# Kernel tuning notes

Measured on AMD Instinct MI355X. Metric: run time of the kernel, lower is better.

Reference implementation:

```python
import jax, jax.numpy as jnp
import numpy as np

EPS = 1e-5
NUM_HEADS = 16


def _layernorm(x, g, b):
    mu = jnp.mean(x, axis=-1, keepdims=True)
    var = jnp.mean(jnp.square(x - mu), axis=-1, keepdims=True)
    return (x - mu) * jax.lax.rsqrt(var + EPS) * g + b


def setup_inputs() -> dict:
    key = jax.random.key(0)
    ks = jax.random.split(key, 8)
    B, N, D, Hid = 2, 2048, 1024, 4096
    s = 0.02
    return {
        "x": jax.random.normal(ks[0], (B, N, D), dtype=jnp.float32),
        "w_qkv": jax.random.normal(ks[1], (D, 3 * D), dtype=jnp.float32) * s,
        "b_qkv": jnp.zeros((3 * D,), dtype=jnp.float32),
        "ln_g": jnp.ones((D,), dtype=jnp.float32),
        "ln_b": jnp.zeros((D,), dtype=jnp.float32),
        "w1": jax.random.normal(ks[2], (D, Hid), dtype=jnp.float32) * s,
        "b1": jnp.zeros((Hid,), dtype=jnp.float32),
        "w2": jax.random.normal(ks[3], (Hid, D), dtype=jnp.float32) * s,
        "b2": jnp.zeros((D,), dtype=jnp.float32),
    }


def reference(x, w_qkv, b_qkv, ln_g, ln_b, w1, b1, w2, b2):
    B, N, D = x.shape
    H = NUM_HEADS
    Dh = D // H

    # --- attention branch (pre-norm, shared LayerNorm params) ---
    xn = _layernorm(x, ln_g, ln_b)
    qkv = xn @ w_qkv + b_qkv                       # [B, N, 3D]
    qkv = qkv.reshape(B, N, 3, H, Dh).transpose(2, 0, 3, 1, 4)  # [3, B, H, N, Dh]
    q, k, v = qkv[0], qkv[1], qkv[2]
    # NOTE: original module applies NO 1/sqrt(Dh) scaling
    att = jax.nn.softmax(jnp.einsum('bhqd,bhkd->bhqk', q, k), axis=-1)
    o = jnp.einsum('bhqk,bhkd->bhqd', att, v)      # [B, H, N, Dh]
    # Faithful to source: raw reshape of [B, H, N, Dh] -> [B, N, D]
    # (the original code does NOT transpose heads back before merging)
    attn_out = o.reshape(B, N, D)
    x = x + attn_out

    # --- MLP branch ---
    xn2 = _layernorm(x, ln_g, ln_b)
    h = jax.nn.gelu(xn2 @ w1 + b1, approximate=False)
    mlp_out = h @ w2 + b2
    return x + mlp_out
```

## Files before the change

### kernel.cpp

```cpp
#include <hip/hip_runtime.h>
#include <cstdint>
#include <math.h>

typedef __attribute__((ext_vector_type(4))) float f32x4;
typedef __attribute__((ext_vector_type(8))) short bf16x8;
typedef unsigned short u16;
typedef __attribute__((ext_vector_type(4))) unsigned short u16x4;

#define LOG2E 1.44269504088896340736f

__device__ __forceinline__ u16 f2bf(float f) {
  uint32_t u = __builtin_bit_cast(uint32_t, f);
  u += 0x7FFFu + ((u >> 16) & 1u);
  return (u16)(u >> 16);
}

__device__ __forceinline__ void g2lds16(const void* g, void* l) {
  __builtin_amdgcn_global_load_lds((const __attribute__((address_space(1))) void*)g,
                                   (__attribute__((address_space(3))) void*)l, 16, 0, 0);
}

__device__ __forceinline__ float qsum16(float v) {
  v += __shfl_xor(v, 1);
  v += __shfl_xor(v, 2);
  v += __shfl_xor(v, 4);
  v += __shfl_xor(v, 8);
  return v;
}
__device__ __forceinline__ float wsum64(float v) {
  #pragma unroll
  for (int m = 32; m > 0; m >>= 1) v += __shfl_xor(v, m);
  return v;
}

__global__ void __launch_bounds__(256) transpose_f32_bf16(
    const float* __restrict__ in, u16* __restrict__ out, int R, int C) {
  __shared__ float tile[32][33];
  const int bx = blockIdx.x, by = blockIdx.y;
  const int tx = threadIdx.x & 31, ty = threadIdx.x >> 5;
  #pragma unroll
  for (int j = 0; j < 4; ++j)
    tile[ty + j * 8][tx] = in[(size_t)(by * 32 + ty + j * 8) * C + bx * 32 + tx];
  __syncthreads();
  #pragma unroll
  for (int j = 0; j < 4; ++j)
    out[(size_t)(bx * 32 + ty + j * 8) * R + by * 32 + tx] = f2bf(tile[tx][ty + j * 8]);
}

__global__ void __launch_bounds__(256) ln_kernel(
    const float* __restrict__ x, const float* __restrict__ g,
    const float* __restrict__ b, u16* __restrict__ out) {
  __shared__ float red[8];
  const int row = blockIdx.x, t = threadIdx.x, w = t >> 6;
  const float4 v = ((const float4*)(x + (size_t)row * 1024))[t];
  float s = v.x + v.y + v.z + v.w;
  s = wsum64(s);
  if ((t & 63) == 0) red[w] = s;
  __syncthreads();
  const float mean = (red[0] + red[1] + red[2] + red[3]) * (1.0f / 1024.0f);
  const float dx = v.x - mean, dy = v.y - mean, dz = v.z - mean, dw = v.w - mean;
  float s2 = dx * dx + dy * dy + dz * dz + dw * dw;
  s2 = wsum64(s2);
  if ((t & 63) == 0) red[4 + w] = s2;
  __syncthreads();
  const float rstd = rsqrtf((red[4] + red[5] + red[6] + red[7]) * (1.0f / 1024.0f) + 1e-5f);
  const float4 gv = ((const float4*)g)[t];
  const float4 bv = ((const float4*)b)[t];
  u16x4 o;
  o.x = f2bf(dx * rstd * gv.x + bv.x);
  o.y = f2bf(dy * rstd * gv.y + bv.y);
  o.z = f2bf(dz * rstd * gv.z + bv.z);
  o.w = f2bf(dw * rstd * gv.w + bv.w);
  ((u16x4*)(out + (size_t)row * 1024))[t] = o;
}

template <int EPI>
__global__ void __launch_bounds__(256, 2) gemm_bt(
    const u16* __restrict__ A, const u16* __restrict__ Bt,
    const float* __restrict__ bias, int M, int N, int K,
    u16* __restrict__ ob, const float* __restrict__ res, float* __restrict__ of) {
  __shared__ u16 As[128 * 32];
  __shared__ u16 Bs[128 * 32];
  const int t = threadIdx.x;
  const int w = t >> 6, l = t & 63;
  const int lq = l >> 4, lr = l & 15;
  const int sw = (lr >> 1) & 3;
  const int wm = w >> 1, wn = w & 1;
  const int row0 = blockIdx.x * 128, col0 = blockIdx.y * 128;
  f32x4 acc[4][4] = {};
  for (int k0 = 0; k0 < K; k0 += 32) {
    #pragma unroll
    for (int i = 0; i < 2; ++i) {
      int c = i * 256 + t;
      int row = c >> 2, cl = (c & 3) ^ ((row >> 1) & 3);
      g2lds16(A + (size_t)(row0 + row) * K + k0 + cl * 8,
              (char*)As + (i * 256 + w * 64) * 16);
    }
    #pragma unroll
    for (int i = 0; i < 2; ++i) {
      int c = i * 256 + t;
      int row = c >> 2, cl = (c & 3) ^ ((row >> 1) & 3);
      g2lds16(Bt + (size_t)(col0 + row) * K + k0 + cl * 8,
              (char*)Bs + (i * 256 + w * 64) * 16);
    }
    __syncthreads();
    bf16x8 af[4], bf[4];
    #pragma unroll
    for (int tm = 0; tm < 4; ++tm)
      af[tm] = *(const bf16x8*)&As[(wm * 64 + tm * 16 + lr) * 32 + (lq ^ sw) * 8];
    #pragma unroll
    for (int tn = 0; tn < 4; ++tn)
      bf[tn] = *(const bf16x8*)&Bs[(wn * 64 + tn * 16 + lr) * 32 + (lq ^ sw) * 8];
    #pragma unroll
    for (int tm = 0; tm < 4; ++tm)
      #pragma unroll
      for (int tn = 0; tn < 4; ++tn)
        acc[tm][tn] = __builtin_amdgcn_mfma_f32_16x16x32_bf16(af[tm], bf[tn], acc[tm][tn], 0, 0, 0);
    __syncthreads();
  }
  #pragma unroll
  for (int tm = 0; tm < 4; ++tm) {
    #pragma unroll
    for (int tn = 0; tn < 4; ++tn) {
      const int gcol = col0 + wn * 64 + tn * 16 + lr;
      const float bv = bias[gcol];
      float vals[4];
      #pragma unroll
      for (int r = 0; r < 4; ++r) vals[r] = acc[tm][tn][r] + bv;
      const int g0 = row0 + wm * 64 + tm * 16 + lq * 4;
      if (EPI == 0) {
        const int tsel = gcol >> 10, hh = (gcol >> 6) & 15, dh = gcol & 63;
        const int bb = g0 >> 11, n0 = g0 & 2047;
        if (tsel == 2) {
          u16x4 pk;
          pk.x = f2bf(vals[0]); pk.y = f2bf(vals[1]);
          pk.z = f2bf(vals[2]); pk.w = f2bf(vals[3]);
          *(u16x4*)&ob[8388608 + (size_t)((bb * 16 + hh) * 64 + dh) * 2048 + n0] = pk;
        } else {
          const float sc = (tsel == 0) ? LOG2E : 1.0f;
          const size_t base = (tsel ? 4194304u : 0u) +
                              (size_t)(bb * 16 + hh) * 2048 * 64 + dh;
          #pragma unroll
          for (int r = 0; r < 4; ++r)
            ob[base + (size_t)(n0 + r) * 64] = f2bf(vals[r] * sc);
        }
      } else if (EPI == 1) {
        #pragma unroll
        for (int r = 0; r < 4; ++r) {
          const float gelu = 0.5f * vals[r] * (1.0f + erff(vals[r] * 0.70710678118654752f));
          ob[(size_t)(g0 + r) * N + gcol] = f2bf(gelu);
        }
      } else {
        #pragma unroll
        for (int r = 0; r < 4; ++r) {
          const size_t idx = (size_t)(g0 + r) * N + gcol;
          of[idx] = res[idx] + vals[r];
        }
      }
    }
  }
}

__global__ void __launch_bounds__(256, 2) attn_kernel(
    const u16* __restrict__ q, const u16* __restrict__ k, const u16* __restrict__ vt,
    const float* __restrict__ x, float* __restrict__ x2) {
  __shared__ u16 Ks[128 * 64];
  __shared__ u16 Vs[64 * 128];
  __shared__ u16 Ps[4][16 * 136];
  const int t = threadIdx.x, w = t >> 6, l = t & 63;
  const int lq = l >> 4, lr = l & 15;
  const int sw = lr & 7;
  const int bh = blockIdx.y, qt = blockIdx.x;
  const size_t head = (size_t)bh * (2048 * 64);
  const u16* qh = q + head;
  const u16* kh = k + head;
  const u16* vth = vt + head;

  bf16x8 qf[2][2];
  #pragma unroll
  for (int tm = 0; tm < 2; ++tm)
    #pragma unroll
    for (int kk = 0; kk < 2; ++kk)
      qf[tm][kk] = *(const bf16x8*)&qh[(size_t)(qt * 128 + w * 32 + tm * 16 + lr) * 64 + kk * 32 + lq * 8];

  f32x4 o_acc[2][4] = {};
  float rsum[2][4] = {};
  u16* const pbase = &Ps[w][lq * 544 + lr];

  for (int kt = 0; kt < 16; ++kt) {
    #pragma unroll
    for (int i = 0; i < 4; ++i) {
      int c = i * 256 + t;
      int row = c >> 3, cl = (c & 7) ^ (row & 7);
      g2lds16(kh + (size_t)(kt * 128 + row) * 64 + cl * 8,
              (char*)Ks + (i * 256 + w * 64) * 16);
    }
    #pragma unroll
    for (int i = 0; i < 4; ++i) {
      int c = i * 256 + t;
      int row = c >> 4, cl = (c & 15) ^ (row & 7);
      g2lds16(vth + (size_t)row * 2048 + kt * 128 + cl * 8,
              (char*)Vs + (i * 256 + w * 64) * 16);
    }
    __syncthreads();
    bf16x8 kf[8][2];
    #pragma unroll
    for (int tn = 0; tn < 8; ++tn)
      #pragma unroll
      for (int kk = 0; kk < 2; ++kk)
        kf[tn][kk] = *(const bf16x8*)&Ks[(tn * 16 + lr) * 64 + ((kk * 4 + lq) ^ sw) * 8];
    #pragma unroll
    for (int tm = 0; tm < 2; ++tm) {
      f32x4 s_acc[8] = {};
      #pragma unroll
      for (int tn = 0; tn < 8; ++tn)
        #pragma unroll
        for (int kk = 0; kk < 2; ++kk)
          s_acc[tn] = __builtin_amdgcn_mfma_f32_16x16x32_bf16(qf[tm][kk], kf[tn][kk], s_acc[tn], 0, 0, 0);
      #pragma unroll
      for (int tn = 0; tn < 8; ++tn)
        #pragma unroll
        for (int r = 0; r < 4; ++r) {
          const float p = __builtin_amdgcn_exp2f(s_acc[tn][r]);
          rsum[tm][r] += p;
          pbase[r * 136 + tn * 16] = (u16)(__builtin_bit_cast(uint32_t, p) >> 16);
        }
      #pragma unroll
      for (int kk2 = 0; kk2 < 4; ++kk2) {
        const bf16x8 pf = *(const bf16x8*)&Ps[w][lr * 136 + kk2 * 32 + lq * 8];
        #pragma unroll
        for (int tn = 0; tn < 4; ++tn) {
          const bf16x8 vf = *(const bf16x8*)&Vs[(tn * 16 + lr) * 128 + ((kk2 * 4 + lq) ^ sw) * 8];
          o_acc[tm][tn] = __builtin_amdgcn_mfma_f32_16x16x32_bf16(pf, vf, o_acc[tm][tn], 0, 0, 0);
        }
      }
    }
    __syncthreads();
  }
  float inv[2][4];
  #pragma unroll
  for (int tm = 0; tm < 2; ++tm)
    #pragma unroll
    for (int r = 0; r < 4; ++r)
      inv[tm][r] = 1.0f / qsum16(rsum[tm][r]);
  const int bb = bh >> 4, hh = bh & 15;
  const size_t base = (size_t)bb * 2097152 + (size_t)hh * 131072;
  #pragma unroll
  for (int tm = 0; tm < 2; ++tm)
    #pragma unroll
    for (int tn = 0; tn < 4; ++tn)
      #pragma unroll
      for (int r = 0; r < 4; ++r) {
        const int n = qt * 128 + w * 32 + tm * 16 + lq * 4 + r;
        const int dh = tn * 16 + lr;
        const size_t idx = base + (size_t)n * 64 + dh;
        x2[idx] = x[idx] + o_acc[tm][tn][r] * inv[tm][r];
      }
}

extern "C" void kernel_launch(void* const* d_in, const int* in_sizes, int n_in,
                              void* d_out, int out_size, void* d_ws, size_t ws_size,
                              hipStream_t stream) {
  const float* x     = (const float*)d_in[0];
  const float* w_qkv = (const float*)d_in[1];
  const float* b_qkv = (const float*)d_in[2];
  const float* ln_g  = (const float*)d_in[3];
  const float* ln_b  = (const float*)d_in[4];
  const float* w1    = (const float*)d_in[5];
  const float* b1    = (const float*)d_in[6];
  const float* w2    = (const float*)d_in[7];
  const float* b2    = (const float*)d_in[8];
  float* out = (float*)d_out;
  char* ws = (char*)d_ws;

  u16*  wqkvT = (u16*)(ws + 0);
  u16*  qb    = (u16*)(ws + 6291456);
  u16*  xn    = (u16*)(ws + 31457280);
  u16*  h     = (u16*)(ws + 0);
  float* x2   = (float*)(ws + 39845888);
  u16*  w1T   = (u16*)(ws + 56623104);
  u16*  w2T   = (u16*)(ws + 65011712);
  u16*  xn2   = (u16*)(ws + 73400320);

  transpose_f32_bf16<<<dim3(3072 / 32, 1024 / 32), 256, 0, stream>>>(w_qkv, wqkvT, 1024, 3072);
  transpose_f32_bf16<<<dim3(4096 / 32, 1024 / 32), 256, 0, stream>>>(w1, w1T, 1024, 4096);
  transpose_f32_bf16<<<dim3(1024 / 32, 4096 / 32), 256, 0, stream>>>(w2, w2T, 4096, 1024);

  ln_kernel<<<4096, 256, 0, stream>>>(x, ln_g, ln_b, xn);
  gemm_bt<0><<<dim3(32, 24), 256, 0, stream>>>(xn, wqkvT, b_qkv, 4096, 3072, 1024,
                                               qb, nullptr, nullptr);
  attn_kernel<<<dim3(16, 32), 256, 0, stream>>>(qb, qb + 4194304, qb + 8388608, x, x2);
  ln_kernel<<<4096, 256, 0, stream>>>(x2, ln_g, ln_b, xn2);
  gemm_bt<1><<<dim3(32, 32), 256, 0, stream>>>(xn2, w1T, b1, 4096, 4096, 1024,
                                               h, nullptr, nullptr);
  gemm_bt<2><<<dim3(32, 8), 256, 0, stream>>>(h, w2T, b2, 4096, 1024, 4096,
                                              nullptr, x2, out);
}
```

Measured before the change: 341.7 us.

## Add double-buffered K=128 GEMM kernel for MLP down-projection

Replaces the generic gemm_bt used for the second MLP matmul (K=4096, N=1024, only 256 blocks) with a dedicated kernel. It stages 128-wide K tiles into two LDS buffers so the next tile's global loads overlap the current tile's MFMA work, and it uses an XOR swizzle suited to the wider tile. The gemm_bt epilogue for the residual case is removed. LDS use rises to 128KB per block, so only one block fits per CU, which lowers occupancy in exchange for fewer barriers and better latency hiding.

```diff
diff --git a/kernel.cpp b/kernel.cpp
--- a/kernel.cpp
+++ b/kernel.cpp
@@ -78,7 +78,7 @@
 __global__ void __launch_bounds__(256, 2) gemm_bt(
     const u16* __restrict__ A, const u16* __restrict__ Bt,
     const float* __restrict__ bias, int M, int N, int K,
-    u16* __restrict__ ob, const float* __restrict__ res, float* __restrict__ of) {
+    u16* __restrict__ ob) {
   __shared__ u16 As[128 * 32];
   __shared__ u16 Bs[128 * 32];
   const int t = threadIdx.x;
@@ -144,18 +144,95 @@
           for (int r = 0; r < 4; ++r)
             ob[base + (size_t)(n0 + r) * 64] = f2bf(vals[r] * sc);
         }
-      } else if (EPI == 1) {
+      } else {
         #pragma unroll
         for (int r = 0; r < 4; ++r) {
           const float gelu = 0.5f * vals[r] * (1.0f + erff(vals[r] * 0.70710678118654752f));
           ob[(size_t)(g0 + r) * N + gcol] = f2bf(gelu);
         }
-      } else {
-        #pragma unroll
-        for (int r = 0; r < 4; ++r) {
-          const size_t idx = (size_t)(g0 + r) * N + gcol;
-          of[idx] = res[idx] + vals[r];
-        }
+      }
+    }
+  }
+}
+
+__global__ void __launch_bounds__(256) gemm2_db(
+    const u16* __restrict__ A, const u16* __restrict__ Bt,
+    const float* __restrict__ bias, const float* __restrict__ res,
+    float* __restrict__ of) {
+  __shared__ u16 As0[128 * 128], As1[128 * 128];
+  __shared__ u16 Bs0[128 * 128], Bs1[128 * 128];
+  const int t = threadIdx.x;
+  const int w = t >> 6, l = t & 63;
+  const int lq = l >> 4, lr = l & 15;
+  const int sw = lr & 7;
+  const int wm = w >> 1, wn = w & 1;
+  const int row0 = blockIdx.x * 128, col0 = blockIdx.y * 128;
+  const int K = 4096, N = 1024;
+
+#define STAGE(kt, AS, BS)                                                  \
+  {                                                                        \
+    _Pragma("unroll")                                                      \
+    for (int i = 0; i < 8; ++i) {                                          \
+      int c = i * 256 + t;                                                 \
+      int row = c >> 4, cl = (c & 15) ^ (row & 7);                         \
+      g2lds16(A + (size_t)(row0 + row) * K + (kt) * 128 + cl * 8,          \
+              (char*)(AS) + (i * 256 + w * 64) * 16);                      \
+    }                                                                      \
+    _Pragma("unroll")                                                      \
+    for (int i = 0; i < 8; ++i) {                                          \
+      int c = i * 256 + t;                                                 \
+      int row = c >> 4, cl = (c & 15) ^ (row & 7);                         \
+      g2lds16(Bt + (size_t)(col0 + row) * K + (kt) * 128 + cl * 8,         \
+              (char*)(BS) + (i * 256 + w * 64) * 16);                      \
+    }                                                                      \
+  }
+
+#define COMPUTE(AS, BS)                                                    \
+  {                                                                        \
+    _Pragma("unroll")                                                      \
+    for (int kk = 0; kk < 4; ++kk) {                                       \
+      bf16x8 af[4], bf[4];                                                 \
+      _Pragma("unroll")                                                    \
+      for (int tm = 0; tm < 4; ++tm)                                       \
+        af[tm] = *(const bf16x8*)&(AS)[(wm * 64 + tm * 16 + lr) * 128 +    \
+                                       (((kk * 4 + lq) ^ sw)) * 8];        \
+      _Pragma("unroll")                                                    \
+      for (int tn = 0; tn < 4; ++tn)                                       \
+        bf[tn] = *(const bf16x8*)&(BS)[(wn * 64 + tn * 16 + lr) * 128 +    \
+                                       (((kk * 4 + lq) ^ sw)) * 8];        \
+      _Pragma("unroll")                                                    \
+      for (int tm = 0; tm < 4; ++tm)                                       \
+        _Pragma("unroll")                                                  \
+        for (int tn = 0; tn < 4; ++tn)                                     \
+          acc[tm][tn] = __builtin_amdgcn_mfma_f32_16x16x32_bf16(           \
+              af[tm], bf[tn], acc[tm][tn], 0, 0, 0);                       \
+    }                                                                      \
+  }
+
+  f32x4 acc[4][4] = {};
+  STAGE(0, As0, Bs0);
+  for (int kt = 0; kt < 32; kt += 2) {
+    __syncthreads();
+    STAGE(kt + 1, As1, Bs1);
+    COMPUTE(As0, Bs0);
+    __syncthreads();
+    if (kt + 2 < 32) STAGE(kt + 2, As0, Bs0);
+    COMPUTE(As1, Bs1);
+  }
+#undef STAGE
+#undef COMPUTE
+
+  #pragma unroll
+  for (int tm = 0; tm < 4; ++tm) {
+    #pragma unroll
+    for (int tn = 0; tn < 4; ++tn) {
+      const int gcol = col0 + wn * 64 + tn * 16 + lr;
+      const float bv = bias[gcol];
+      const int g0 = row0 + wm * 64 + tm * 16 + lq * 4;
+      #pragma unroll
+      for (int r = 0; r < 4; ++r) {
+        const size_t idx = (size_t)(g0 + r) * N + gcol;
+        of[idx] = res[idx] + acc[tm][tn][r] + bv;
       }
     }
   }
@@ -287,12 +364,9 @@
   transpose_f32_bf16<<<dim3(1024 / 32, 4096 / 32), 256, 0, stream>>>(w2, w2T, 4096, 1024);
 
   ln_kernel<<<4096, 256, 0, stream>>>(x, ln_g, ln_b, xn);
-  gemm_bt<0><<<dim3(32, 24), 256, 0, stream>>>(xn, wqkvT, b_qkv, 4096, 3072, 1024,
-                                               qb, nullptr, nullptr);
+  gemm_bt<0><<<dim3(32, 24), 256, 0, stream>>>(xn, wqkvT, b_qkv, 4096, 3072, 1024, qb);
   attn_kernel<<<dim3(16, 32), 256, 0, stream>>>(qb, qb + 4194304, qb + 8388608, x, x2);
   ln_kernel<<<4096, 256, 0, stream>>>(x2, ln_g, ln_b, xn2);
-  gemm_bt<1><<<dim3(32, 32), 256, 0, stream>>>(xn2, w1T, b1, 4096, 4096, 1024,
-                                               h, nullptr, nullptr);
-  gemm_bt<2><<<dim3(32, 8), 256, 0, stream>>>(h, w2T, b2, 4096, 1024, 4096,
-                                              nullptr, x2, out);
-}
+  gemm_bt<1><<<dim3(32, 32), 256, 0, stream>>>(xn2, w1T, b1, 4096, 4096, 1024, h);
+  gemm2_db<<<dim3(32, 8), 256, 0, stream>>>(h, w2T, b2, x2, out);
+}
```

Result: faster. 318.8 us (-6.7%).
